# Performance work log

Hardware: AMD Instinct MI355X
Metric: run time of the kernel (lower is better)

## Reference

```python
import jax, jax.numpy as jnp
import numpy as np

B_, T_, TS, DE, H, LD, OD = 16, 4096, 64, 128, 256, 512, 10
RMIN, RMAX, MAXPH = 0.9, 0.999, 6.283
EPS = 1e-5
NBLK = 6


def setup_inputs() -> dict:
    key = jax.random.key(0)
    ks = jax.random.split(key, 14)
    x = jax.random.normal(ks[0], (B_, T_, TS), jnp.float32)
    # LRU ring init (Orvieto et al.)
    u1 = jax.random.uniform(ks[1], (NBLK, H))
    u2 = jax.random.uniform(ks[2], (NBLK, H))
    nu_log = jnp.log(-0.5 * jnp.log(u1 * (RMAX**2 - RMIN**2) + RMIN**2))
    theta_log = jnp.log(MAXPH * u2)
    B_re = jax.random.normal(ks[3], (NBLK, H, DE)) / np.sqrt(2 * DE)
    B_im = jax.random.normal(ks[4], (NBLK, H, DE)) / np.sqrt(2 * DE)
    C_re = jax.random.normal(ks[5], (NBLK, DE, H)) / np.sqrt(H)
    C_im = jax.random.normal(ks[6], (NBLK, DE, H)) / np.sqrt(H)
    D_lru = jax.random.normal(ks[7], (NBLK, DE))
    W1 = jax.random.normal(ks[8], (NBLK, DE, LD)) / np.sqrt(DE)
    b1 = jnp.zeros((NBLK, LD))
    W2 = jax.random.normal(ks[9], (NBLK, LD // 2, DE)) / np.sqrt(LD // 2)
    b2 = jnp.zeros((NBLK, DE))
    bn_scale = jnp.ones((NBLK, DE))
    bn_bias = jnp.zeros((NBLK, DE))
    W_enc = jax.random.normal(ks[10], (TS, DE)) / np.sqrt(TS)
    b_enc = jnp.zeros((DE,))
    W_out = jax.random.normal(ks[11], (DE, OD)) / np.sqrt(DE)
    b_out = jnp.zeros((OD,))
    return dict(x=x, nu_log=nu_log, theta_log=theta_log, B_re=B_re, B_im=B_im,
                C_re=C_re, C_im=C_im, D_lru=D_lru, W1=W1, b1=b1, W2=W2, b2=b2,
                bn_scale=bn_scale, bn_bias=bn_bias, W_enc=W_enc, b_enc=b_enc,
                W_out=W_out, b_out=b_out)


def _lru(u, nu_log_i, theta_log_i, Bre, Bim, Cre, Cim, Dv):
    # u: [B,T,DE] float. Diagonal complex linear recurrence via associative scan.
    lam = jnp.exp(-jnp.exp(nu_log_i) + 1j * jnp.exp(theta_log_i))        # [H]
    gamma = jnp.sqrt(jnp.clip(1.0 - jnp.abs(lam) ** 2, 1e-8, None))      # [H]
    Bc = (Bre + 1j * Bim) * gamma[:, None]                               # [H,DE]
    Bu = jnp.einsum('btd,hd->bth', u.astype(jnp.complex64), Bc)          # [B,T,H]
    lam_b = jnp.broadcast_to(lam, Bu.shape)

    def binop(a, b):
        return (a[0] * b[0], a[1] * b[0] + b[1])

    _, h = jax.lax.associative_scan(binop, (lam_b, Bu), axis=1)          # [B,T,H]
    y = jnp.einsum('bth,dh->btd', h, Cre + 1j * Cim).real + u * Dv
    return y


def _bn(x, scale, bias):
    # training-mode batchnorm over (batch, time) with feature axis last
    m = x.mean(axis=(0, 1))
    v = x.var(axis=(0, 1))
    return (x - m) * jax.lax.rsqrt(v + EPS) * scale + bias


def reference(x, nu_log, theta_log, B_re, B_im, C_re, C_im, D_lru,
              W1, b1, W2, b2, bn_scale, bn_bias, W_enc, b_enc, W_out, b_out):
    h = x @ W_enc + b_enc                       # [B,T,DE]
    y = h
    for i in range(NBLK):
        z = _bn(h, bn_scale[i], bn_bias[i])
        z = _lru(z, nu_log[i], theta_log[i], B_re[i], B_im[i], C_re[i], C_im[i], D_lru[i])
        z = z @ W1[i] + b1[i]                   # [B,T,LD]
        a, b = jnp.split(z, 2, axis=-1)
        z = a * jax.nn.sigmoid(b)               # GLU
        z = z @ W2[i] + b2[i]                   # [B,T,DE]
        h = z + y                               # residual to encoder output
    pooled = h.mean(axis=1)                     # pool=True: mean over tokens
    return pooled @ W_out + b_out               # [B,OD]
```

## Files before the change

kernel.cpp:

```cpp
#include <hip/hip_runtime.h>
#include <hip/hip_fp16.h>

#define BB 16
#define TT 4096
#define TSZ 64
#define DE 128
#define HH 256
#define LDIM 512
#define ODIM 10
#define NBLKS 6
#define EPSF 1e-5f
#define NC32 128
#define NROWS (BB*TT)

typedef _Float16 f16x8 __attribute__((ext_vector_type(8)));
typedef _Float16 f16x4 __attribute__((ext_vector_type(4)));
typedef float f32x4 __attribute__((ext_vector_type(4)));
#define MFMA16(a,b,c) __builtin_amdgcn_mfma_f32_16x16x32_f16((a),(b),(c),0,0,0)

enum : size_t {
  HOFF_BG = 0,
  HOFF_WC = HOFF_BG + (size_t)NBLKS*512*128,
  HOFF_W1 = HOFF_WC + (size_t)NBLKS*128*512,
  HOFF_W2 = HOFF_W1 + (size_t)NBLKS*512*128,
  HOFF_WE = HOFF_W2 + (size_t)NBLKS*128*256,
  HTOT_HALFS = HOFF_WE + 128*64
};

enum : size_t {
  WOFF_Y     = 0,
  WOFF_H     = WOFF_Y + (size_t)NROWS*DE/2,
  WOFF_W16   = WOFF_H + (size_t)NROWS*DE/2,
  WOFF_LAM   = WOFF_W16 + (HTOT_HALFS+1)/2,
  WOFF_LAML  = WOFF_LAM + (size_t)NBLKS*HH*2,
  WOFF_SL    = WOFF_LAML + (size_t)NBLKS*HH*2,
  WOFF_CARRY = WOFF_SL + (size_t)BB*NC32*HH*2,
  WOFF_STATS = WOFF_CARRY + (size_t)BB*NC32*HH*2,
  WOFF_POOL  = WOFF_STATS + (size_t)(NBLKS+1)*2*DE,
  WOFF_BU    = WOFF_POOL + (size_t)BB*DE,
  WS_FLOATS  = WOFF_BU + (size_t)BB*NC32*512*32/2
};

__global__ __launch_bounds__(256) void k_prep(
    const float* __restrict__ nu_log, const float* __restrict__ theta_log,
    const float* __restrict__ B_re, const float* __restrict__ B_im,
    const float* __restrict__ C_re, const float* __restrict__ C_im,
    const float* __restrict__ W1g, const float* __restrict__ W2g,
    const float* __restrict__ Wenc, float* __restrict__ ws)
{
  const int i = blockIdx.x, h = threadIdx.x;
  __half* w16 = (__half*)(ws + WOFF_W16);
  const float nu  = expf(nu_log[i*HH+h]);
  const float th  = expf(theta_log[i*HH+h]);
  const float mod = expf(-nu);
  const float lr = mod*cosf(th), li = mod*sinf(th);
  const float gamma = sqrtf(fmaxf(1.0f - mod*mod, 1e-8f));
  ws[WOFF_LAM + ((size_t)i*HH+h)*2+0] = lr;
  ws[WOFF_LAM + ((size_t)i*HH+h)*2+1] = li;
  {
    float ar = lr, ai = li;
    #pragma unroll
    for (int q = 0; q < 5; q++) { float nr=ar*ar-ai*ai, ni=2.0f*ar*ai; ar=nr; ai=ni; }
    ws[WOFF_LAML + ((size_t)i*HH+h)*2+0] = ar;
    ws[WOFF_LAML + ((size_t)i*HH+h)*2+1] = ai;
  }
  {
    __half* bg = w16 + HOFF_BG + (size_t)i*512*128;
    const float* bre = B_re + ((size_t)i*HH+h)*DE;
    const float* bim = B_im + ((size_t)i*HH+h)*DE;
    for (int d = 0; d < DE; d++) {
      bg[(size_t)h*128 + d]       = __float2half(bre[d]*gamma);
      bg[(size_t)(256+h)*128 + d] = __float2half(bim[d]*gamma);
    }
  }
  {
    __half* wc = w16 + HOFF_WC + (size_t)i*128*512;
    const float* cre = C_re + (size_t)i*DE*HH;
    const float* cim = C_im + (size_t)i*DE*HH;
    for (int d = 0; d < DE; d++) {
      wc[(size_t)d*512 + 2*h]     = __float2half( cre[(size_t)d*HH + h]);
      wc[(size_t)d*512 + 2*h + 1] = __float2half(-cim[(size_t)d*HH + h]);
    }
  }
  {
    __half* w1t = w16 + HOFF_W1 + (size_t)i*512*128;
    for (int d = 0; d < DE; d++) {
      w1t[(size_t)h*128 + d]       = __float2half(W1g[((size_t)i*DE + d)*LDIM + h]);
      w1t[(size_t)(256+h)*128 + d] = __float2half(W1g[((size_t)i*DE + d)*LDIM + 256 + h]);
    }
  }
  if (h < 128) {
    __half* w2t = w16 + HOFF_W2 + (size_t)i*128*256;
    for (int g = 0; g < 256; g++)
      w2t[(size_t)h*256 + g] = __float2half(W2g[((size_t)i*256 + g)*DE + h]);
  }
  if (i == 0 && h < 128) {
    __half* wet = w16 + HOFF_WE;
    for (int k = 0; k < TSZ; k++)
      wet[(size_t)h*TSZ + k] = __float2half(Wenc[(size_t)k*DE + h]);
  }
}

__global__ __launch_bounds__(512) void k_enc(
    const float* __restrict__ x, const float* __restrict__ benc, float* __restrict__ ws)
{
  __shared__ __half XT[64*72];
  __shared__ __half YS[64*136];
  const int tid = threadIdx.x, w = tid >> 6, l = tid & 63;
  const size_t row0 = (size_t)blockIdx.x * 64;
  {
    const float4* xg = (const float4*)(x + row0*TSZ);
    for (int idx = tid; idx < 1024; idx += 512) {
      float4 v = xg[idx];
      const int r = idx >> 4, c4 = (idx & 15)*4;
      *(__half2*)&XT[r*72 + c4]     = __half2{__float2half(v.x), __float2half(v.y)};
      *(__half2*)&XT[r*72 + c4 + 2] = __half2{__float2half(v.z), __float2half(v.w)};
    }
  }
  __syncthreads();
  const __half* wet = (const __half*)(ws + WOFF_W16) + HOFF_WE;
  const int n0 = w*16;
  f32x4 acc[4];
  #pragma unroll
  for (int mt = 0; mt < 4; mt++) acc[mt] = (f32x4)(0.0f);
  #pragma unroll
  for (int k0 = 0; k0 < 64; k0 += 32) {
    f16x8 bf = *(const f16x8*)&wet[(size_t)(n0 + (l&15))*64 + k0 + (l>>4)*8];
    #pragma unroll
    for (int mt = 0; mt < 4; mt++) {
      f16x8 af = *(const f16x8*)&XT[(mt*16 + (l&15))*72 + k0 + (l>>4)*8];
      acc[mt] = MFMA16(af, bf, acc[mt]);
    }
  }
  const int d = n0 + (l&15);
  const float be = benc[d];
  float s = 0.0f, ss = 0.0f;
  #pragma unroll
  for (int mt = 0; mt < 4; mt++)
    #pragma unroll
    for (int j = 0; j < 4; j++) {
      const int t = mt*16 + (l>>4)*4 + j;
      const float v = acc[mt][j] + be;
      YS[t*136 + d] = __float2half(v);
      s += v; ss += v*v;
    }
  s  += __shfl_xor(s, 16);  s  += __shfl_xor(s, 32);
  ss += __shfl_xor(ss, 16); ss += __shfl_xor(ss, 32);
  if (l < 16) {
    atomicAdd(ws + WOFF_STATS + d, s);
    atomicAdd(ws + WOFF_STATS + DE + d, ss);
  }
  __syncthreads();
  __half* y = (__half*)(ws + WOFF_Y);
  const int row = tid >> 3, d0 = (tid & 7)*16;
  *(f16x8*)&y[(row0+row)*DE + d0]     = *(const f16x8*)&YS[row*136 + d0];
  *(f16x8*)&y[(row0+row)*DE + d0 + 8] = *(const f16x8*)&YS[row*136 + d0 + 8];
}

__global__ __launch_bounds__(512, 4) void k_A(
    const __half* __restrict__ hin, float* __restrict__ ws,
    const float* __restrict__ bnsg, const float* __restrict__ bnbg, int iblk)
{
  __shared__ __half U[32*136];
  __shared__ __half BU[32*520];
  __shared__ float AC[256];
  const int tid = threadIdx.x, w = tid >> 6, l = tid & 63, q = l >> 4, r = l & 15;
  const int b = blockIdx.y, cbg = blockIdx.x;
  const int h = tid & 255;
  if (tid < 128) {
    const float inv = 1.0f / (float)NROWS;
    const float s  = ws[WOFF_STATS + ((size_t)iblk*2+0)*DE + tid];
    const float sq = ws[WOFF_STATS + ((size_t)iblk*2+1)*DE + tid];
    const float mean = s*inv;
    const float var  = sq*inv - mean*mean;
    const float a = rsqrtf(var + EPSF) * bnsg[iblk*DE + tid];
    AC[tid]       = a;
    AC[128 + tid] = bnbg[iblk*DE + tid] - mean*a;
  }
  const __half* BG = (const __half*)(ws + WOFF_W16) + HOFF_BG + (size_t)iblk*512*128;
  const int n0 = w*64;
  const float lr = ws[WOFF_LAM + ((size_t)iblk*HH+h)*2+0];
  const float li = ws[WOFF_LAM + ((size_t)iblk*HH+h)*2+1];
  f16x8 bg4[4][4];
  #pragma unroll
  for (int nt = 0; nt < 4; nt++)
    #pragma unroll
    for (int k = 0; k < 4; k++)
      bg4[nt][k] = *(const f16x8*)&BG[(size_t)(n0 + nt*16 + r)*128 + k*32 + q*8];
  __half* bug = (__half*)(ws + WOFF_BU);
  __syncthreads();

  for (int it = 0; it < 4; it++) {
    const int cb = cbg*4 + it;
    const int row0 = b*TT + cb*32;
    {
      const int row = tid >> 4, d0 = (tid & 15)*8;
      f16x8 hv = *(const f16x8*)(hin + (size_t)(row0+row)*DE + d0);
      f16x8 uv;
      #pragma unroll
      for (int j = 0; j < 8; j++)
        uv[j] = (_Float16)((float)hv[j]*AC[d0+j] + AC[128+d0+j]);
      *(f16x8*)&U[row*136 + d0] = uv;
    }
    __syncthreads();
    {
      f32x4 acc[2][4];
      #pragma unroll
      for (int mt = 0; mt < 2; mt++)
        #pragma unroll
        for (int nt = 0; nt < 4; nt++) acc[mt][nt] = (f32x4)(0.0f);
      #pragma unroll
      for (int k = 0; k < 4; k++) {
        f16x8 af0 = *(const f16x8*)&U[(r)*136      + k*32 + q*8];
        f16x8 af1 = *(const f16x8*)&U[(16 + r)*136 + k*32 + q*8];
        #pragma unroll
        for (int nt = 0; nt < 4; nt++) {
          acc[0][nt] = MFMA16(af0, bg4[nt][k], acc[0][nt]);
          acc[1][nt] = MFMA16(af1, bg4[nt][k], acc[1][nt]);
        }
      }
      #pragma unroll
      for (int mt = 0; mt < 2; mt++)
        #pragma unroll
        for (int nt = 0; nt < 4; nt++) {
          f16x4 pk;
          #pragma unroll
          for (int j = 0; j < 4; j++) {
            pk[j] = (_Float16)acc[mt][nt][j];
            BU[(mt*16 + q*4 + j)*520 + n0 + nt*16 + r] = __float2half(acc[mt][nt][j]);
          }
          const int hc = n0 + nt*16 + r;
          *(f16x4*)(bug + (((size_t)(b*NC32 + cb)*512 + hc)*32 + mt*16 + q*4)) = pk;
        }
    }
    __syncthreads();
    if (tid < 256) {
      float sr = 0.0f, si = 0.0f;
      #pragma unroll
      for (int t = 0; t < 32; t++) {
        const float br = (float)BU[t*520 + h];
        const float bi = (float)BU[t*520 + 256 + h];
        const float nr = lr*sr - li*si + br;
        const float ni = lr*si + li*sr + bi;
        sr = nr; si = ni;
      }
      *((float2*)(ws + WOFF_SL) + ((size_t)b*NC32 + cb)*HH + h) = float2{sr, si};
    }
    __syncthreads();
  }
}

__global__ void k_carry(float* __restrict__ ws, int i)
{
  const int b = blockIdx.x >> 2;
  const int h = (blockIdx.x & 3)*64 + threadIdx.x;
  const float Lr = ws[WOFF_LAML + ((size_t)i*HH+h)*2+0];
  const float Li = ws[WOFF_LAML + ((size_t)i*HH+h)*2+1];
  float2* C = (float2*)(ws + WOFF_CARRY) + (size_t)b*NC32*HH + h;
  const float2* S = (const float2*)(ws + WOFF_SL) + (size_t)b*NC32*HH + h;
  float sr = 0.0f, si = 0.0f;
  C[0] = float2{0.0f, 0.0f};
  for (int c0 = 0; c0 < 120; c0 += 8) {
    float2 sl[8];
    #pragma unroll
    for (int j = 0; j < 8; j++) sl[j] = S[(size_t)(c0+j)*HH];
    #pragma unroll
    for (int j = 0; j < 8; j++) {
      const float nr = Lr*sr - Li*si + sl[j].x;
      const float ni = Lr*si + Li*sr + sl[j].y;
      sr = nr; si = ni;
      C[(size_t)(c0+j+1)*HH] = float2{sr, si};
    }
  }
  {
    float2 sl[7];
    #pragma unroll
    for (int j = 0; j < 7; j++) sl[j] = S[(size_t)(120+j)*HH];
    #pragma unroll
    for (int j = 0; j < 7; j++) {
      const float nr = Lr*sr - Li*si + sl[j].x;
      const float ni = Lr*si + Li*sr + sl[j].y;
      sr = nr; si = ni;
      C[(size_t)(121+j)*HH] = float2{sr, si};
    }
  }
}

__global__ __launch_bounds__(512, 4) void k_BC(
    const __half* __restrict__ hin, float* __restrict__ ws,
    const float* __restrict__ bnsg, const float* __restrict__ bnbg,
    const float* __restrict__ b1g, const float* __restrict__ b2g,
    const float* __restrict__ Dvg, int iblk, int islast)
{
  __shared__ __half U[32*136];
  __shared__ __half HT[32*520];
  __shared__ __half YL[32*136];
  __shared__ __half YR[32*136];
  __shared__ float AC[256];
  __shared__ float DVs[128];
  const int tid = threadIdx.x, w = tid >> 6, l = tid & 63, q = l >> 4, r = l & 15;
  const int b = blockIdx.y, cbg = blockIdx.x;
  const __half* w16 = (const __half*)(ws + WOFF_W16);
  const int d = w*16 + r;
  const int h = tid & 255;

  if (tid < 128) {
    const float inv = 1.0f / (float)NROWS;
    const float s  = ws[WOFF_STATS + ((size_t)iblk*2+0)*DE + tid];
    const float sq = ws[WOFF_STATS + ((size_t)iblk*2+1)*DE + tid];
    const float mean = s*inv;
    const float var  = sq*inv - mean*mean;
    const float a = rsqrtf(var + EPSF) * bnsg[iblk*DE + tid];
    AC[tid]       = a;
    AC[128 + tid] = bnbg[iblk*DE + tid] - mean*a;
    DVs[tid] = Dvg[iblk*DE + tid];
  }

  const float lr = ws[WOFF_LAM + ((size_t)iblk*HH+h)*2+0];
  const float li = ws[WOFF_LAM + ((size_t)iblk*HH+h)*2+1];
  float b1a[2], b1b[2];
  #pragma unroll
  for (int nt = 0; nt < 2; nt++) {
    const int ca = w*32 + nt*16 + r;
    b1a[nt] = b1g[(size_t)iblk*LDIM + ca];
    b1b[nt] = b1g[(size_t)iblk*LDIM + 256 + ca];
  }
  const float bb2 = b2g[(size_t)iblk*DE + d];
  const __half* WC  = w16 + HOFF_WC + (size_t)iblk*128*512;
  const __half* W1T = w16 + HOFF_W1 + (size_t)iblk*512*128;
  const __half* W2T = w16 + HOFF_W2 + (size_t)iblk*128*256;
  const __half* bug = (const __half*)(ws + WOFF_BU);
  const __half* yh = (const __half*)(ws + WOFF_Y);
  __half* hh = (__half*)(ws + WOFF_H);
  float s_acc = 0.0f, ss_acc = 0.0f;
  __syncthreads();

  for (int it = 0; it < 4; it++) {
    const int cb = cbg*4 + it;
    const int row0 = b*TT + cb*32;

    {
      const int row = tid >> 4, d0 = (tid & 15)*8;
      f16x8 hv  = *(const f16x8*)(hin + (size_t)(row0+row)*DE + d0);
      f16x8 yv8 = *(const f16x8*)(yh  + (size_t)(row0+row)*DE + d0);
      f16x8 uv;
      #pragma unroll
      for (int j = 0; j < 8; j++)
        uv[j] = (_Float16)((float)hv[j]*AC[d0+j] + AC[128+d0+j]);
      *(f16x8*)&U[row*136 + d0]  = uv;
      *(f16x8*)&YR[row*136 + d0] = yv8;
    }
    if (tid < 256) {
      const __half* bu = bug + ((size_t)(b*NC32 + cb)*512)*32;
      f16x8 bre[4], bim[4];
      #pragma unroll
      for (int k = 0; k < 4; k++) {
        bre[k] = *(const f16x8*)(bu + (size_t)h*32 + k*8);
        bim[k] = *(const f16x8*)(bu + (size_t)(256+h)*32 + k*8);
      }
      const float2 carry = *((const float2*)(ws + WOFF_CARRY) + ((size_t)b*NC32 + cb)*HH + h);
      float sr = carry.x, si = carry.y;
      #pragma unroll
      for (int t = 0; t < 32; t++) {
        const float br = (float)bre[t>>3][t&7];
        const float bi = (float)bim[t>>3][t&7];
        const float nr = lr*sr - li*si + br;
        const float ni = lr*si + li*sr + bi;
        sr = nr; si = ni;
        *(__half2*)&HT[t*520 + 2*h] = __half2{__float2half(sr), __float2half(si)};
      }
    }
    __syncthreads();

    {
      f16x8 wc[16];
      #pragma unroll
      for (int k = 0; k < 16; k++)
        wc[k] = *(const f16x8*)&WC[(size_t)d*512 + k*32 + q*8];
      f32x4 a0 = (f32x4)(0.0f), a1 = (f32x4)(0.0f);
      #pragma unroll
      for (int k = 0; k < 16; k++) {
        f16x8 af0 = *(const f16x8*)&HT[(r)*520      + k*32 + q*8];
        f16x8 af1 = *(const f16x8*)&HT[(16 + r)*520 + k*32 + q*8];
        a0 = MFMA16(af0, wc[k], a0);
        a1 = MFMA16(af1, wc[k], a1);
      }
      const float dv = DVs[d];
      #pragma unroll
      for (int mt = 0; mt < 2; mt++)
        #pragma unroll
        for (int j = 0; j < 4; j++) {
          const int t = mt*16 + q*4 + j;
          const float u = (float)U[t*136 + d];
          YL[t*136 + d] = __float2half((mt ? a1[j] : a0[j]) + u*dv);
        }
    }
    __syncthreads();

    {
      #pragma unroll
      for (int nt = 0; nt < 2; nt++) {
        const int ca = w*32 + nt*16 + r;
        f16x8 wa[4], wb[4];
        #pragma unroll
        for (int k = 0; k < 4; k++) {
          wa[k] = *(const f16x8*)&W1T[(size_t)ca*128 + k*32 + q*8];
          wb[k] = *(const f16x8*)&W1T[(size_t)(256+ca)*128 + k*32 + q*8];
        }
        f32x4 aa0 = (f32x4)(0.0f), aa1 = (f32x4)(0.0f);
        f32x4 ab0 = (f32x4)(0.0f), ab1 = (f32x4)(0.0f);
        #pragma unroll
        for (int k = 0; k < 4; k++) {
          f16x8 af0 = *(const f16x8*)&YL[(r)*136      + k*32 + q*8];
          f16x8 af1 = *(const f16x8*)&YL[(16 + r)*136 + k*32 + q*8];
          aa0 = MFMA16(af0, wa[k], aa0);
          aa1 = MFMA16(af1, wa[k], aa1);
          ab0 = MFMA16(af0, wb[k], ab0);
          ab1 = MFMA16(af1, wb[k], ab1);
        }
        #pragma unroll
        for (int mt = 0; mt < 2; mt++)
          #pragma unroll
          for (int j = 0; j < 4; j++) {
            const int t = mt*16 + q*4 + j;
            const float av = (mt ? aa1[j] : aa0[j]) + b1a[nt];
            const float bv = (mt ? ab1[j] : ab0[j]) + b1b[nt];
            HT[t*520 + ca] = __float2half(av / (1.0f + __expf(-bv)));
          }
      }
    }
    __syncthreads();

    {
      f16x8 w2f[8];
      #pragma unroll
      for (int k = 0; k < 8; k++)
        w2f[k] = *(const f16x8*)&W2T[(size_t)d*256 + k*32 + q*8];
      f32x4 a0 = (f32x4)(0.0f), a1 = (f32x4)(0.0f);
      #pragma unroll
      for (int k = 0; k < 8; k++) {
        f16x8 af0 = *(const f16x8*)&HT[(r)*520      + k*32 + q*8];
        f16x8 af1 = *(const f16x8*)&HT[(16 + r)*520 + k*32 + q*8];
        a0 = MFMA16(af0, w2f[k], a0);
        a1 = MFMA16(af1, w2f[k], a1);
      }
      #pragma unroll
      for (int mt = 0; mt < 2; mt++)
        #pragma unroll
        for (int j = 0; j < 4; j++) {
          const int t = mt*16 + q*4 + j;
          const float v = (mt ? a1[j] : a0[j]) + bb2 + (float)YR[t*136 + d];
          YR[t*136 + d] = __float2half(v);
          s_acc += v; ss_acc += v*v;
        }
    }
    __syncthreads();

    {
      const int row = tid >> 4, d0 = (tid & 15)*8;
      *(f16x8*)(hh + (size_t)(row0+row)*DE + d0) = *(const f16x8*)&YR[row*136 + d0];
    }
    __syncthreads();
  }

  s_acc  += __shfl_xor(s_acc, 16);  s_acc  += __shfl_xor(s_acc, 32);
  ss_acc += __shfl_xor(ss_acc, 16); ss_acc += __shfl_xor(ss_acc, 32);
  if (l < 16) {
    atomicAdd(ws + WOFF_STATS + (size_t)((iblk+1)*2 + 0)*DE + d, s_acc);
    atomicAdd(ws + WOFF_STATS + (size_t)((iblk+1)*2 + 1)*DE + d, ss_acc);
    if (islast) atomicAdd(ws + WOFF_POOL + (size_t)b*DE + d, s_acc);
  }
}

__global__ void k_out(const float* __restrict__ Wout, const float* __restrict__ bout,
                      const float* __restrict__ ws, float* __restrict__ out)
{
  const int tid = threadIdx.x;
  if (tid < BB*ODIM) {
    const int b = tid / ODIM, o = tid % ODIM;
    float acc = bout[o];
    const float* p = ws + WOFF_POOL + (size_t)b*DE;
    const float invT = 1.0f / (float)TT;
    for (int d = 0; d < DE; d++) acc += p[d]*invT*Wout[d*ODIM + o];
    out[tid] = acc;
  }
}

extern "C" void kernel_launch(void* const* d_in, const int* in_sizes, int n_in,
                              void* d_out, int out_size, void* d_ws, size_t ws_size,
                              hipStream_t stream)
{
  const float* x   = (const float*)d_in[0];
  const float* nu  = (const float*)d_in[1];
  const float* th  = (const float*)d_in[2];
  const float* Bre = (const float*)d_in[3];
  const float* Bim = (const float*)d_in[4];
  const float* Cre = (const float*)d_in[5];
  const float* Cim = (const float*)d_in[6];
  const float* Dv  = (const float*)d_in[7];
  const float* W1  = (const float*)d_in[8];
  const float* b1  = (const float*)d_in[9];
  const float* W2  = (const float*)d_in[10];
  const float* b2  = (const float*)d_in[11];
  const float* bns = (const float*)d_in[12];
  const float* bnb = (const float*)d_in[13];
  const float* We  = (const float*)d_in[14];
  const float* be  = (const float*)d_in[15];
  const float* Wo  = (const float*)d_in[16];
  const float* bo  = (const float*)d_in[17];
  float* ws = (float*)d_ws;
  float* out = (float*)d_out;

  hipMemsetAsync(ws + WOFF_STATS, 0,
                 (size_t)(((NBLKS+1)*2*DE) + BB*DE)*sizeof(float), stream);

  k_prep<<<NBLKS, 256, 0, stream>>>(nu, th, Bre, Bim, Cre, Cim, W1, W2, We, ws);
  k_enc<<<NROWS/64, 512, 0, stream>>>(x, be, ws);

  const __half* Yh = (const __half*)(ws + WOFF_Y);
  const __half* Hh = (const __half*)(ws + WOFF_H);
  for (int i = 0; i < NBLKS; i++) {
    const __half* hin = (i == 0) ? Yh : Hh;
    k_A    <<<dim3(32, BB), 512, 0, stream>>>(hin, ws, bns, bnb, i);
    k_carry<<<64, 64, 0, stream>>>(ws, i);
    k_BC   <<<dim3(32, BB), 512, 0, stream>>>(hin, ws, bns, bnb, b1, b2, Dv, i,
                                              (i == NBLKS-1) ? 1 : 0);
  }
  k_out<<<1, 256, 0, stream>>>(Wo, bo, ws, out);
}
```

Before: 901.0 us.

## Process 64-row tiles in k_BC with split real/imag C projection

k_BC now handles two 32-step chunks per iteration (64 rows), so each loaded weight fragment feeds four MFMA row tiles instead of two, and all 512 threads run the scan replay instead of half. The C weights are stored with real and imaginary halves split, so the state tile only needs to hold 256 columns. It does the real pass, then overwrites the tile with imaginary parts kept in registers and does a second pass, which costs one extra barrier round. Shared memory padding strides change (SU, SH, BU stride 536) to cut bank conflicts, and the residual buffer reuses U so the LDS footprint stays similar while register pressure grows.

```diff
diff --git a/kernel.cpp b/kernel.cpp
--- a/kernel.cpp
+++ b/kernel.cpp
@@ -41,6 +41,9 @@
   WS_FLOATS  = WOFF_BU + (size_t)BB*NC32*512*32/2
 };
 
+#define SU 152
+#define SH 280
+
 __global__ __launch_bounds__(256) void k_prep(
     const float* __restrict__ nu_log, const float* __restrict__ theta_log,
     const float* __restrict__ B_re, const float* __restrict__ B_im,
@@ -78,8 +81,8 @@
     const float* cre = C_re + (size_t)i*DE*HH;
     const float* cim = C_im + (size_t)i*DE*HH;
     for (int d = 0; d < DE; d++) {
-      wc[(size_t)d*512 + 2*h]     = __float2half( cre[(size_t)d*HH + h]);
-      wc[(size_t)d*512 + 2*h + 1] = __float2half(-cim[(size_t)d*HH + h]);
+      wc[(size_t)d*512 + h]       = __float2half( cre[(size_t)d*HH + h]);
+      wc[(size_t)d*512 + 256 + h] = __float2half(-cim[(size_t)d*HH + h]);
     }
   }
   {
@@ -162,7 +165,7 @@
     const float* __restrict__ bnsg, const float* __restrict__ bnbg, int iblk)
 {
   __shared__ __half U[32*136];
-  __shared__ __half BU[32*520];
+  __shared__ __half BU[32*536];
   __shared__ float AC[256];
   const int tid = threadIdx.x, w = tid >> 6, l = tid & 63, q = l >> 4, r = l & 15;
   const int b = blockIdx.y, cbg = blockIdx.x;
@@ -227,7 +230,7 @@
           #pragma unroll
           for (int j = 0; j < 4; j++) {
             pk[j] = (_Float16)acc[mt][nt][j];
-            BU[(mt*16 + q*4 + j)*520 + n0 + nt*16 + r] = __float2half(acc[mt][nt][j]);
+            BU[(mt*16 + q*4 + j)*536 + n0 + nt*16 + r] = __float2half(acc[mt][nt][j]);
           }
           const int hc = n0 + nt*16 + r;
           *(f16x4*)(bug + (((size_t)(b*NC32 + cb)*512 + hc)*32 + mt*16 + q*4)) = pk;
@@ -238,8 +241,8 @@
       float sr = 0.0f, si = 0.0f;
       #pragma unroll
       for (int t = 0; t < 32; t++) {
-        const float br = (float)BU[t*520 + h];
-        const float bi = (float)BU[t*520 + 256 + h];
+        const float br = (float)BU[t*536 + h];
+        const float bi = (float)BU[t*536 + 256 + h];
         const float nr = lr*sr - li*si + br;
         const float ni = lr*si + li*sr + bi;
         sr = nr; si = ni;
@@ -292,17 +295,16 @@
     const float* __restrict__ b1g, const float* __restrict__ b2g,
     const float* __restrict__ Dvg, int iblk, int islast)
 {
-  __shared__ __half U[32*136];
-  __shared__ __half HT[32*520];
-  __shared__ __half YL[32*136];
-  __shared__ __half YR[32*136];
+  __shared__ __half U[64*SU];
+  __shared__ __half HT[64*SH];
+  __shared__ __half YL[64*SU];
   __shared__ float AC[256];
   __shared__ float DVs[128];
   const int tid = threadIdx.x, w = tid >> 6, l = tid & 63, q = l >> 4, r = l & 15;
   const int b = blockIdx.y, cbg = blockIdx.x;
   const __half* w16 = (const __half*)(ws + WOFF_W16);
   const int d = w*16 + r;
-  const int h = tid & 255;
+  const int h = tid & 255, cl = tid >> 8;
 
   if (tid < 128) {
     const float inv = 1.0f / (float)NROWS;
@@ -335,22 +337,29 @@
   float s_acc = 0.0f, ss_acc = 0.0f;
   __syncthreads();
 
-  for (int it = 0; it < 4; it++) {
-    const int cb = cbg*4 + it;
-    const int row0 = b*TT + cb*32;
-
-    {
-      const int row = tid >> 4, d0 = (tid & 15)*8;
-      f16x8 hv  = *(const f16x8*)(hin + (size_t)(row0+row)*DE + d0);
-      f16x8 yv8 = *(const f16x8*)(yh  + (size_t)(row0+row)*DE + d0);
-      f16x8 uv;
-      #pragma unroll
-      for (int j = 0; j < 8; j++)
-        uv[j] = (_Float16)((float)hv[j]*AC[d0+j] + AC[128+d0+j]);
-      *(f16x8*)&U[row*136 + d0]  = uv;
-      *(f16x8*)&YR[row*136 + d0] = yv8;
-    }
-    if (tid < 256) {
+  for (int it = 0; it < 2; it++) {
+    const int cb0 = cbg*4 + it*2;
+    const int row0 = b*TT + cb0*32;
+
+    f16x8 yv0, yv1;
+    {
+      const int row = tid >> 3, d0 = (tid & 7)*16;
+      const __half* hp = hin + (size_t)(row0+row)*DE + d0;
+      f16x8 h0 = *(const f16x8*)hp, h1 = *(const f16x8*)(hp+8);
+      yv0 = *(const f16x8*)(yh + (size_t)(row0+row)*DE + d0);
+      yv1 = *(const f16x8*)(yh + (size_t)(row0+row)*DE + d0 + 8);
+      f16x8 u0, u1;
+      #pragma unroll
+      for (int j = 0; j < 8; j++) {
+        u0[j] = (_Float16)((float)h0[j]*AC[d0+j]   + AC[128+d0+j]);
+        u1[j] = (_Float16)((float)h1[j]*AC[d0+8+j] + AC[128+d0+8+j]);
+      }
+      *(f16x8*)&U[row*SU + d0]     = u0;
+      *(f16x8*)&U[row*SU + d0 + 8] = u1;
+    }
+    f16x8 si8[4];
+    {
+      const int cb = cb0 + cl;
       const __half* bu = bug + ((size_t)(b*NC32 + cb)*512)*32;
       f16x8 bre[4], bim[4];
       #pragma unroll
@@ -367,36 +376,62 @@
         const float nr = lr*sr - li*si + br;
         const float ni = lr*si + li*sr + bi;
         sr = nr; si = ni;
-        *(__half2*)&HT[t*520 + 2*h] = __half2{__float2half(sr), __float2half(si)};
+        HT[(cl*32 + t)*SH + h] = __float2half(sr);
+        si8[t>>3][t&7] = (_Float16)si;
       }
     }
     __syncthreads();
 
-    {
-      f16x8 wc[16];
-      #pragma unroll
-      for (int k = 0; k < 16; k++)
-        wc[k] = *(const f16x8*)&WC[(size_t)d*512 + k*32 + q*8];
-      f32x4 a0 = (f32x4)(0.0f), a1 = (f32x4)(0.0f);
-      #pragma unroll
-      for (int k = 0; k < 16; k++) {
-        f16x8 af0 = *(const f16x8*)&HT[(r)*520      + k*32 + q*8];
-        f16x8 af1 = *(const f16x8*)&HT[(16 + r)*520 + k*32 + q*8];
-        a0 = MFMA16(af0, wc[k], a0);
-        a1 = MFMA16(af1, wc[k], a1);
-      }
+    f32x4 acc[4];
+    #pragma unroll
+    for (int mt = 0; mt < 4; mt++) acc[mt] = (f32x4)(0.0f);
+    {
+      f16x8 wcre[8];
+      #pragma unroll
+      for (int k = 0; k < 8; k++)
+        wcre[k] = *(const f16x8*)&WC[(size_t)d*512 + k*32 + q*8];
+      #pragma unroll
+      for (int k = 0; k < 8; k++)
+        #pragma unroll
+        for (int mt = 0; mt < 4; mt++) {
+          f16x8 af = *(const f16x8*)&HT[(mt*16 + r)*SH + k*32 + q*8];
+          acc[mt] = MFMA16(af, wcre[k], acc[mt]);
+        }
+    }
+    __syncthreads();
+    #pragma unroll
+    for (int t = 0; t < 32; t++)
+      HT[(cl*32 + t)*SH + h] = si8[t>>3][t&7];
+    __syncthreads();
+    {
+      f16x8 wcim[8];
+      #pragma unroll
+      for (int k = 0; k < 8; k++)
+        wcim[k] = *(const f16x8*)&WC[(size_t)d*512 + 256 + k*32 + q*8];
+      #pragma unroll
+      for (int k = 0; k < 8; k++)
+        #pragma unroll
+        for (int mt = 0; mt < 4; mt++) {
+          f16x8 af = *(const f16x8*)&HT[(mt*16 + r)*SH + k*32 + q*8];
+          acc[mt] = MFMA16(af, wcim[k], acc[mt]);
+        }
       const float dv = DVs[d];
       #pragma unroll
-      for (int mt = 0; mt < 2; mt++)
+      for (int mt = 0; mt < 4; mt++)
         #pragma unroll
         for (int j = 0; j < 4; j++) {
           const int t = mt*16 + q*4 + j;
-          const float u = (float)U[t*136 + d];
-          YL[t*136 + d] = __float2half((mt ? a1[j] : a0[j]) + u*dv);
-        }
-    }
-    __syncthreads();
-
+          const float u = (float)U[t*SU + d];
+          YL[t*SU + d] = __float2half(acc[mt][j] + u*dv);
+        }
+    }
+    __syncthreads();
+
+    {
+      const int row = tid >> 3, d0 = (tid & 7)*16;
+      *(f16x8*)&U[row*SU + d0]     = yv0;
+      *(f16x8*)&U[row*SU + d0 + 8] = yv1;
+    }
     {
       #pragma unroll
       for (int nt = 0; nt < 2; nt++) {
@@ -407,25 +442,25 @@
           wa[k] = *(const f16x8*)&W1T[(size_t)ca*128 + k*32 + q*8];
           wb[k] = *(const f16x8*)&W1T[(size_t)(256+ca)*128 + k*32 + q*8];
         }
-        f32x4 aa0 = (f32x4)(0.0f), aa1 = (f32x4)(0.0f);
-        f32x4 ab0 = (f32x4)(0.0f), ab1 = (f32x4)(0.0f);
-        #pragma unroll
-        for (int k = 0; k < 4; k++) {
-          f16x8 af0 = *(const f16x8*)&YL[(r)*136      + k*32 + q*8];
-          f16x8 af1 = *(const f16x8*)&YL[(16 + r)*136 + k*32 + q*8];
-          aa0 = MFMA16(af0, wa[k], aa0);
-          aa1 = MFMA16(af1, wa[k], aa1);
-          ab0 = MFMA16(af0, wb[k], ab0);
-          ab1 = MFMA16(af1, wb[k], ab1);
-        }
-        #pragma unroll
-        for (int mt = 0; mt < 2; mt++)
+        f32x4 aa[4], ab[4];
+        #pragma unroll
+        for (int mt = 0; mt < 4; mt++) { aa[mt] = (f32x4)(0.0f); ab[mt] = (f32x4)(0.0f); }
+        #pragma unroll
+        for (int k = 0; k < 4; k++)
+          #pragma unroll
+          for (int mt = 0; mt < 4; mt++) {
+            f16x8 af = *(const f16x8*)&YL[(mt*16 + r)*SU + k*32 + q*8];
+            aa[mt] = MFMA16(af, wa[k], aa[mt]);
+            ab[mt] = MFMA16(af, wb[k], ab[mt]);
+          }
+        #pragma unroll
+        for (int mt = 0; mt < 4; mt++)
           #pragma unroll
           for (int j = 0; j < 4; j++) {
             const int t = mt*16 + q*4 + j;
-            const float av = (mt ? aa1[j] : aa0[j]) + b1a[nt];
-            const float bv = (mt ? ab1[j] : ab0[j]) + b1b[nt];
-            HT[t*520 + ca] = __float2half(av / (1.0f + __expf(-bv)));
+            const float av = aa[mt][j] + b1a[nt];
+            const float bv = ab[mt][j] + b1b[nt];
+            HT[t*SH + ca] = __float2half(av / (1.0f + __expf(-bv)));
           }
       }
     }
@@ -436,29 +471,32 @@
       #pragma unroll
       for (int k = 0; k < 8; k++)
         w2f[k] = *(const f16x8*)&W2T[(size_t)d*256 + k*32 + q*8];
-      f32x4 a0 = (f32x4)(0.0f), a1 = (f32x4)(0.0f);
-      #pragma unroll
-      for (int k = 0; k < 8; k++) {
-        f16x8 af0 = *(const f16x8*)&HT[(r)*520      + k*32 + q*8];
-        f16x8 af1 = *(const f16x8*)&HT[(16 + r)*520 + k*32 + q*8];
-        a0 = MFMA16(af0, w2f[k], a0);
-        a1 = MFMA16(af1, w2f[k], a1);
-      }
-      #pragma unroll
-      for (int mt = 0; mt < 2; mt++)
+      f32x4 a2[4];
+      #pragma unroll
+      for (int mt = 0; mt < 4; mt++) a2[mt] = (f32x4)(0.0f);
+      #pragma unroll
+      for (int k = 0; k < 8; k++)
+        #pragma unroll
+        for (int mt = 0; mt < 4; mt++) {
+          f16x8 af = *(const f16x8*)&HT[(mt*16 + r)*SH + k*32 + q*8];
+          a2[mt] = MFMA16(af, w2f[k], a2[mt]);
+        }
+      #pragma unroll
+      for (int mt = 0; mt < 4; mt++)
         #pragma unroll
         for (int j = 0; j < 4; j++) {
           const int t = mt*16 + q*4 + j;
-          const float v = (mt ? a1[j] : a0[j]) + bb2 + (float)YR[t*136 + d];
-          YR[t*136 + d] = __float2half(v);
+          const float v = a2[mt][j] + bb2 + (float)U[t*SU + d];
+          U[t*SU + d] = __float2half(v);
           s_acc += v; ss_acc += v*v;
         }
     }
     __syncthreads();
 
     {
-      const int row = tid >> 4, d0 = (tid & 15)*8;
-      *(f16x8*)(hh + (size_t)(row0+row)*DE + d0) = *(const f16x8*)&YR[row*136 + d0];
+      const int row = tid >> 3, d0 = (tid & 7)*16;
+      *(f16x8*)(hh + (size_t)(row0+row)*DE + d0)     = *(const f16x8*)&U[row*SU + d0];
+      *(f16x8*)(hh + (size_t)(row0+row)*DE + d0 + 8) = *(const f16x8*)&U[row*SU + d0 + 8];
     }
     __syncthreads();
   }
```

Result: faster. 883.3 us (-2.0%).

## Shrink k_BC to 256 threads with split real/imag LDS staging

Applied to the files above, without the earlier changes.

Reworks k_BC to use 256-thread blocks over a doubled grid, each covering two 32-row chunks instead of four. The LDS footprint is cut by staging the real and imaginary scan states separately through a 280-wide buffer, with the imaginary part kept in registers between two MFMA passes. The YR buffer is dropped by reusing U, and the C weight layout changes from interleaved re/im to separate halves. The goal is higher occupancy and more blocks in flight per CU, at the cost of extra barriers and more register pressure for the held imaginary values.

```diff
diff --git a/kernel.cpp b/kernel.cpp
--- a/kernel.cpp
+++ b/kernel.cpp
@@ -41,6 +41,8 @@
   WS_FLOATS  = WOFF_BU + (size_t)BB*NC32*512*32/2
 };
 
+#define SH2 280
+
 __global__ __launch_bounds__(256) void k_prep(
     const float* __restrict__ nu_log, const float* __restrict__ theta_log,
     const float* __restrict__ B_re, const float* __restrict__ B_im,
@@ -78,8 +80,8 @@
     const float* cre = C_re + (size_t)i*DE*HH;
     const float* cim = C_im + (size_t)i*DE*HH;
     for (int d = 0; d < DE; d++) {
-      wc[(size_t)d*512 + 2*h]     = __float2half( cre[(size_t)d*HH + h]);
-      wc[(size_t)d*512 + 2*h + 1] = __float2half(-cim[(size_t)d*HH + h]);
+      wc[(size_t)d*512 + h]       = __float2half( cre[(size_t)d*HH + h]);
+      wc[(size_t)d*512 + 256 + h] = __float2half(-cim[(size_t)d*HH + h]);
     }
   }
   {
@@ -162,7 +164,7 @@
     const float* __restrict__ bnsg, const float* __restrict__ bnbg, int iblk)
 {
   __shared__ __half U[32*136];
-  __shared__ __half BU[32*520];
+  __shared__ __half BU[32*536];
   __shared__ float AC[256];
   const int tid = threadIdx.x, w = tid >> 6, l = tid & 63, q = l >> 4, r = l & 15;
   const int b = blockIdx.y, cbg = blockIdx.x;
@@ -227,7 +229,7 @@
           #pragma unroll
           for (int j = 0; j < 4; j++) {
             pk[j] = (_Float16)acc[mt][nt][j];
-            BU[(mt*16 + q*4 + j)*520 + n0 + nt*16 + r] = __float2half(acc[mt][nt][j]);
+            BU[(mt*16 + q*4 + j)*536 + n0 + nt*16 + r] = __float2half(acc[mt][nt][j]);
           }
           const int hc = n0 + nt*16 + r;
           *(f16x4*)(bug + (((size_t)(b*NC32 + cb)*512 + hc)*32 + mt*16 + q*4)) = pk;
@@ -238,8 +240,8 @@
       float sr = 0.0f, si = 0.0f;
       #pragma unroll
       for (int t = 0; t < 32; t++) {
-        const float br = (float)BU[t*520 + h];
-        const float bi = (float)BU[t*520 + 256 + h];
+        const float br = (float)BU[t*536 + h];
+        const float bi = (float)BU[t*536 + 256 + h];
         const float nr = lr*sr - li*si + br;
         const float ni = lr*si + li*sr + bi;
         sr = nr; si = ni;
@@ -286,23 +288,21 @@
   }
 }
 
-__global__ __launch_bounds__(512, 4) void k_BC(
+__global__ __launch_bounds__(256, 4) void k_BC(
     const __half* __restrict__ hin, float* __restrict__ ws,
     const float* __restrict__ bnsg, const float* __restrict__ bnbg,
     const float* __restrict__ b1g, const float* __restrict__ b2g,
     const float* __restrict__ Dvg, int iblk, int islast)
 {
   __shared__ __half U[32*136];
-  __shared__ __half HT[32*520];
+  __shared__ __half HT[32*SH2];
   __shared__ __half YL[32*136];
-  __shared__ __half YR[32*136];
   __shared__ float AC[256];
   __shared__ float DVs[128];
   const int tid = threadIdx.x, w = tid >> 6, l = tid & 63, q = l >> 4, r = l & 15;
   const int b = blockIdx.y, cbg = blockIdx.x;
   const __half* w16 = (const __half*)(ws + WOFF_W16);
-  const int d = w*16 + r;
-  const int h = tid & 255;
+  const int h = tid;
 
   if (tid < 128) {
     const float inv = 1.0f / (float)NROWS;
@@ -318,157 +318,206 @@
 
   const float lr = ws[WOFF_LAM + ((size_t)iblk*HH+h)*2+0];
   const float li = ws[WOFF_LAM + ((size_t)iblk*HH+h)*2+1];
-  float b1a[2], b1b[2];
+  float bb2[2];
   #pragma unroll
-  for (int nt = 0; nt < 2; nt++) {
-    const int ca = w*32 + nt*16 + r;
-    b1a[nt] = b1g[(size_t)iblk*LDIM + ca];
-    b1b[nt] = b1g[(size_t)iblk*LDIM + 256 + ca];
-  }
-  const float bb2 = b2g[(size_t)iblk*DE + d];
+  for (int nt = 0; nt < 2; nt++)
+    bb2[nt] = b2g[(size_t)iblk*DE + w*32 + nt*16 + r];
   const __half* WC  = w16 + HOFF_WC + (size_t)iblk*128*512;
   const __half* W1T = w16 + HOFF_W1 + (size_t)iblk*512*128;
   const __half* W2T = w16 + HOFF_W2 + (size_t)iblk*128*256;
   const __half* bug = (const __half*)(ws + WOFF_BU);
   const __half* yh = (const __half*)(ws + WOFF_Y);
   __half* hh = (__half*)(ws + WOFF_H);
-  float s_acc = 0.0f, ss_acc = 0.0f;
+  float s_acc[2] = {0.0f, 0.0f}, ss_acc[2] = {0.0f, 0.0f};
   __syncthreads();
 
-  for (int it = 0; it < 4; it++) {
-    const int cb = cbg*4 + it;
+  for (int it = 0; it < 2; it++) {
+    const int cb = cbg*2 + it;
     const int row0 = b*TT + cb*32;
-
-    {
-      const int row = tid >> 4, d0 = (tid & 15)*8;
-      f16x8 hv  = *(const f16x8*)(hin + (size_t)(row0+row)*DE + d0);
-      f16x8 yv8 = *(const f16x8*)(yh  + (size_t)(row0+row)*DE + d0);
-      f16x8 uv;
-      #pragma unroll
-      for (int j = 0; j < 8; j++)
-        uv[j] = (_Float16)((float)hv[j]*AC[d0+j] + AC[128+d0+j]);
-      *(f16x8*)&U[row*136 + d0]  = uv;
-      *(f16x8*)&YR[row*136 + d0] = yv8;
-    }
-    if (tid < 256) {
+    const int rr = tid >> 4, dd0 = (tid & 15)*8;
+
+    {
+      f16x8 h0 = *(const f16x8*)(hin + (size_t)(row0+rr)*DE + dd0);
+      f16x8 h1 = *(const f16x8*)(hin + (size_t)(row0+16+rr)*DE + dd0);
+      f16x8 u0, u1;
+      #pragma unroll
+      for (int j = 0; j < 8; j++) {
+        u0[j] = (_Float16)((float)h0[j]*AC[dd0+j] + AC[128+dd0+j]);
+        u1[j] = (_Float16)((float)h1[j]*AC[dd0+j] + AC[128+dd0+j]);
+      }
+      *(f16x8*)&U[rr*136 + dd0]      = u0;
+      *(f16x8*)&U[(16+rr)*136 + dd0] = u1;
+    }
+    f16x8 si8[4];
+    {
       const __half* bu = bug + ((size_t)(b*NC32 + cb)*512)*32;
-      f16x8 bre[4], bim[4];
-      #pragma unroll
-      for (int k = 0; k < 4; k++) {
-        bre[k] = *(const f16x8*)(bu + (size_t)h*32 + k*8);
-        bim[k] = *(const f16x8*)(bu + (size_t)(256+h)*32 + k*8);
-      }
       const float2 carry = *((const float2*)(ws + WOFF_CARRY) + ((size_t)b*NC32 + cb)*HH + h);
       float sr = carry.x, si = carry.y;
-      #pragma unroll
-      for (int t = 0; t < 32; t++) {
-        const float br = (float)bre[t>>3][t&7];
-        const float bi = (float)bim[t>>3][t&7];
-        const float nr = lr*sr - li*si + br;
-        const float ni = lr*si + li*sr + bi;
-        sr = nr; si = ni;
-        *(__half2*)&HT[t*520 + 2*h] = __half2{__float2half(sr), __float2half(si)};
-      }
-    }
-    __syncthreads();
-
-    {
-      f16x8 wc[16];
-      #pragma unroll
-      for (int k = 0; k < 16; k++)
-        wc[k] = *(const f16x8*)&WC[(size_t)d*512 + k*32 + q*8];
-      f32x4 a0 = (f32x4)(0.0f), a1 = (f32x4)(0.0f);
-      #pragma unroll
-      for (int k = 0; k < 16; k++) {
-        f16x8 af0 = *(const f16x8*)&HT[(r)*520      + k*32 + q*8];
-        f16x8 af1 = *(const f16x8*)&HT[(16 + r)*520 + k*32 + q*8];
-        a0 = MFMA16(af0, wc[k], a0);
-        a1 = MFMA16(af1, wc[k], a1);
-      }
-      const float dv = DVs[d];
+      f16x8 rc = *(const f16x8*)(bu + (size_t)h*32);
+      f16x8 ic = *(const f16x8*)(bu + (size_t)(256+h)*32);
+      #pragma unroll
+      for (int g = 0; g < 4; g++) {
+        f16x8 rn, im_n;
+        if (g < 3) {
+          rn   = *(const f16x8*)(bu + (size_t)h*32 + (g+1)*8);
+          im_n = *(const f16x8*)(bu + (size_t)(256+h)*32 + (g+1)*8);
+        }
+        #pragma unroll
+        for (int j = 0; j < 8; j++) {
+          const float br = (float)rc[j];
+          const float bi = (float)ic[j];
+          const float nr = lr*sr - li*si + br;
+          const float ni = lr*si + li*sr + bi;
+          sr = nr; si = ni;
+          HT[(g*8 + j)*SH2 + h] = __float2half(sr);
+          si8[g][j] = (_Float16)si;
+        }
+        rc = rn; ic = im_n;
+      }
+    }
+    __syncthreads();
+
+    f32x4 acc[2][2];
+    #pragma unroll
+    for (int mt = 0; mt < 2; mt++)
+      #pragma unroll
+      for (int nt = 0; nt < 2; nt++) acc[mt][nt] = (f32x4)(0.0f);
+    #pragma unroll
+    for (int k = 0; k < 8; k++) {
+      f16x8 af0 = *(const f16x8*)&HT[(r)*SH2      + k*32 + q*8];
+      f16x8 af1 = *(const f16x8*)&HT[(16 + r)*SH2 + k*32 + q*8];
+      #pragma unroll
+      for (int nt = 0; nt < 2; nt++) {
+        f16x8 bf = *(const f16x8*)&WC[(size_t)(w*32 + nt*16 + r)*512 + k*32 + q*8];
+        acc[0][nt] = MFMA16(af0, bf, acc[0][nt]);
+        acc[1][nt] = MFMA16(af1, bf, acc[1][nt]);
+      }
+    }
+    __syncthreads();
+    #pragma unroll
+    for (int g = 0; g < 4; g++)
+      #pragma unroll
+      for (int j = 0; j < 8; j++)
+        HT[(g*8 + j)*SH2 + h] = si8[g][j];
+    __syncthreads();
+    #pragma unroll
+    for (int k = 0; k < 8; k++) {
+      f16x8 af0 = *(const f16x8*)&HT[(r)*SH2      + k*32 + q*8];
+      f16x8 af1 = *(const f16x8*)&HT[(16 + r)*SH2 + k*32 + q*8];
+      #pragma unroll
+      for (int nt = 0; nt < 2; nt++) {
+        f16x8 bf = *(const f16x8*)&WC[(size_t)(w*32 + nt*16 + r)*512 + 256 + k*32 + q*8];
+        acc[0][nt] = MFMA16(af0, bf, acc[0][nt]);
+        acc[1][nt] = MFMA16(af1, bf, acc[1][nt]);
+      }
+    }
+    #pragma unroll
+    for (int nt = 0; nt < 2; nt++) {
+      const int d2 = w*32 + nt*16 + r;
+      const float dv = DVs[d2];
       #pragma unroll
       for (int mt = 0; mt < 2; mt++)
         #pragma unroll
         for (int j = 0; j < 4; j++) {
           const int t = mt*16 + q*4 + j;
-          const float u = (float)U[t*136 + d];
-          YL[t*136 + d] = __float2half((mt ? a1[j] : a0[j]) + u*dv);
-        }
-    }
-    __syncthreads();
-
-    {
+          const float u = (float)U[t*136 + d2];
+          YL[t*136 + d2] = __float2half(acc[mt][nt][j] + u*dv);
+        }
+    }
+    __syncthreads();
+
+    {
+      f16x8 y0 = *(const f16x8*)(yh + (size_t)(row0+rr)*DE + dd0);
+      f16x8 y1 = *(const f16x8*)(yh + (size_t)(row0+16+rr)*DE + dd0);
+      *(f16x8*)&U[rr*136 + dd0]      = y0;
+      *(f16x8*)&U[(16+rr)*136 + dd0] = y1;
+    }
+    #pragma unroll
+    for (int p = 0; p < 4; p++) {
+      const int ca = w*64 + p*16 + r;
+      f16x8 wa[4], wb[4];
+      #pragma unroll
+      for (int k = 0; k < 4; k++) {
+        wa[k] = *(const f16x8*)&W1T[(size_t)ca*128 + k*32 + q*8];
+        wb[k] = *(const f16x8*)&W1T[(size_t)(256+ca)*128 + k*32 + q*8];
+      }
+      f32x4 aa[2], ab[2];
+      aa[0] = aa[1] = (f32x4)(0.0f);
+      ab[0] = ab[1] = (f32x4)(0.0f);
+      #pragma unroll
+      for (int k = 0; k < 4; k++) {
+        f16x8 af0 = *(const f16x8*)&YL[(r)*136      + k*32 + q*8];
+        f16x8 af1 = *(const f16x8*)&YL[(16 + r)*136 + k*32 + q*8];
+        aa[0] = MFMA16(af0, wa[k], aa[0]);
+        aa[1] = MFMA16(af1, wa[k], aa[1]);
+        ab[0] = MFMA16(af0, wb[k], ab[0]);
+        ab[1] = MFMA16(af1, wb[k], ab[1]);
+      }
+      const float b1a = b1g[(size_t)iblk*LDIM + ca];
+      const float b1b = b1g[(size_t)iblk*LDIM + 256 + ca];
+      #pragma unroll
+      for (int mt = 0; mt < 2; mt++)
+        #pragma unroll
+        for (int j = 0; j < 4; j++) {
+          const int t = mt*16 + q*4 + j;
+          const float av = aa[mt][j] + b1a;
+          const float bv = ab[mt][j] + b1b;
+          HT[t*SH2 + ca] = __float2half(av / (1.0f + __expf(-bv)));
+        }
+    }
+    __syncthreads();
+
+    {
+      f32x4 a2[2][2];
+      #pragma unroll
+      for (int mt = 0; mt < 2; mt++)
+        #pragma unroll
+        for (int nt = 0; nt < 2; nt++) a2[mt][nt] = (f32x4)(0.0f);
+      #pragma unroll
+      for (int k = 0; k < 8; k++) {
+        f16x8 af0 = *(const f16x8*)&HT[(r)*SH2      + k*32 + q*8];
+        f16x8 af1 = *(const f16x8*)&HT[(16 + r)*SH2 + k*32 + q*8];
+        #pragma unroll
+        for (int nt = 0; nt < 2; nt++) {
+          f16x8 bf = *(const f16x8*)&W2T[(size_t)(w*32 + nt*16 + r)*256 + k*32 + q*8];
+          a2[0][nt] = MFMA16(af0, bf, a2[0][nt]);
+          a2[1][nt] = MFMA16(af1, bf, a2[1][nt]);
+        }
+      }
       #pragma unroll
       for (int nt = 0; nt < 2; nt++) {
-        const int ca = w*32 + nt*16 + r;
-        f16x8 wa[4], wb[4];
-        #pragma unroll
-        for (int k = 0; k < 4; k++) {
-          wa[k] = *(const f16x8*)&W1T[(size_t)ca*128 + k*32 + q*8];
-          wb[k] = *(const f16x8*)&W1T[(size_t)(256+ca)*128 + k*32 + q*8];
-        }
-        f32x4 aa0 = (f32x4)(0.0f), aa1 = (f32x4)(0.0f);
-        f32x4 ab0 = (f32x4)(0.0f), ab1 = (f32x4)(0.0f);
-        #pragma unroll
-        for (int k = 0; k < 4; k++) {
-          f16x8 af0 = *(const f16x8*)&YL[(r)*136      + k*32 + q*8];
-          f16x8 af1 = *(const f16x8*)&YL[(16 + r)*136 + k*32 + q*8];
-          aa0 = MFMA16(af0, wa[k], aa0);
-          aa1 = MFMA16(af1, wa[k], aa1);
-          ab0 = MFMA16(af0, wb[k], ab0);
-          ab1 = MFMA16(af1, wb[k], ab1);
-        }
+        const int d2 = w*32 + nt*16 + r;
         #pragma unroll
         for (int mt = 0; mt < 2; mt++)
           #pragma unroll
           for (int j = 0; j < 4; j++) {
             const int t = mt*16 + q*4 + j;
-            const float av = (mt ? aa1[j] : aa0[j]) + b1a[nt];
-            const float bv = (mt ? ab1[j] : ab0[j]) + b1b[nt];
-            HT[t*520 + ca] = __float2half(av / (1.0f + __expf(-bv)));
+            const float v = a2[mt][nt][j] + bb2[nt] + (float)U[t*136 + d2];
+            U[t*136 + d2] = __float2half(v);
+            s_acc[nt] += v; ss_acc[nt] += v*v;
           }
       }
     }
     __syncthreads();
 
     {
-      f16x8 w2f[8];
-      #pragma unroll
-      for (int k = 0; k < 8; k++)
-        w2f[k] = *(const f16x8*)&W2T[(size_t)d*256 + k*32 + q*8];
-      f32x4 a0 = (f32x4)(0.0f), a1 = (f32x4)(0.0f);
-      #pragma unroll
-      for (int k = 0; k < 8; k++) {
-        f16x8 af0 = *(const f16x8*)&HT[(r)*520      + k*32 + q*8];
-        f16x8 af1 = *(const f16x8*)&HT[(16 + r)*520 + k*32 + q*8];
-        a0 = MFMA16(af0, w2f[k], a0);
-        a1 = MFMA16(af1, w2f[k], a1);
-      }
-      #pragma unroll
-      for (int mt = 0; mt < 2; mt++)
-        #pragma unroll
-        for (int j = 0; j < 4; j++) {
-          const int t = mt*16 + q*4 + j;
-          const float v = (mt ? a1[j] : a0[j]) + bb2 + (float)YR[t*136 + d];
-          YR[t*136 + d] = __float2half(v);
-          s_acc += v; ss_acc += v*v;
-        }
-    }
-    __syncthreads();
-
-    {
-      const int row = tid >> 4, d0 = (tid & 15)*8;
-      *(f16x8*)(hh + (size_t)(row0+row)*DE + d0) = *(const f16x8*)&YR[row*136 + d0];
-    }
-    __syncthreads();
-  }
-
-  s_acc  += __shfl_xor(s_acc, 16);  s_acc  += __shfl_xor(s_acc, 32);
-  ss_acc += __shfl_xor(ss_acc, 16); ss_acc += __shfl_xor(ss_acc, 32);
-  if (l < 16) {
-    atomicAdd(ws + WOFF_STATS + (size_t)((iblk+1)*2 + 0)*DE + d, s_acc);
-    atomicAdd(ws + WOFF_STATS + (size_t)((iblk+1)*2 + 1)*DE + d, ss_acc);
-    if (islast) atomicAdd(ws + WOFF_POOL + (size_t)b*DE + d, s_acc);
+      *(f16x8*)(hh + (size_t)(row0+rr)*DE + dd0)      = *(const f16x8*)&U[rr*136 + dd0];
+      *(f16x8*)(hh + (size_t)(row0+16+rr)*DE + dd0)   = *(const f16x8*)&U[(16+rr)*136 + dd0];
+    }
+    __syncthreads();
+  }
+
+  #pragma unroll
+  for (int nt = 0; nt < 2; nt++) {
+    float s = s_acc[nt], ss = ss_acc[nt];
+    s  += __shfl_xor(s, 16);  s  += __shfl_xor(s, 32);
+    ss += __shfl_xor(ss, 16); ss += __shfl_xor(ss, 32);
+    if (l < 16) {
+      const int d2 = w*32 + nt*16 + l;
+      atomicAdd(ws + WOFF_STATS + (size_t)((iblk+1)*2 + 0)*DE + d2, s);
+      atomicAdd(ws + WOFF_STATS + (size_t)((iblk+1)*2 + 1)*DE + d2, ss);
+      if (islast) atomicAdd(ws + WOFF_POOL + (size_t)b*DE + d2, s);
+    }
   }
 }
 
@@ -523,7 +572,7 @@
     const __half* hin = (i == 0) ? Yh : Hh;
     k_A    <<<dim3(32, BB), 512, 0, stream>>>(hin, ws, bns, bnb, i);
     k_carry<<<64, 64, 0, stream>>>(ws, i);
-    k_BC   <<<dim3(32, BB), 512, 0, stream>>>(hin, ws, bns, bnb, b1, b2, Dv, i,
+    k_BC   <<<dim3(64, BB), 256, 0, stream>>>(hin, ws, bns, bnb, b1, b2, Dv, i,
                                               (i == NBLKS-1) ? 1 : 0);
   }
   k_out<<<1, 256, 0, stream>>>(Wo, bo, ws, out);
```

Result: slower. 1.069 ms (+18.6%).
